# Performance work log

Hardware: AMD Instinct MI355X
Metric: run time of the kernel (lower is better)

The kernel has to match this reference:

```python
import jax, jax.numpy as jnp
import numpy as np
from jax import lax

STRIDE = (1, 1)
PADDING = (1, 1)


def setup_inputs() -> dict:
    key = jax.random.key(0)
    k1, k2 = jax.random.split(key)
    x = jax.random.normal(k1, (32, 128, 56, 56), dtype=jnp.float32)
    kernels = jax.random.normal(k2, (256, 128, 3, 3), dtype=jnp.float32)
    return {"x": x, "kernels": kernels}


def reference(x, kernels):
    # Equivalent to the python-loop correlation conv: NCHW input, OIHW weight,
    # cross-correlation (no kernel flip), stride/padding per module config.
    out = lax.conv_general_dilated(
        x, kernels,
        window_strides=STRIDE,
        padding=[(PADDING[0], PADDING[0]), (PADDING[1], PADDING[1])],
        dimension_numbers=("NCHW", "OIHW", "NCHW"),
    )
    return out
```

## Files before the change

### kernel.cpp

```cpp
#include <hip/hip_runtime.h>
#include <cstdint>

#define N_IMG 32
#define C_IN 128
#define H_IN 56
#define W_IN 56
#define K_OUT 256
#define HW (H_IN * W_IN)
#define M_TOTAL (N_IMG * HW)
#define XP_H 58
#define XP_W 58
#define XP_ELEMS (N_IMG * XP_H * XP_W * C_IN)
#define WT_ELEMS (9 * K_OUT * C_IN)
#define NKT 36

typedef __bf16 bf16x8 __attribute__((ext_vector_type(8)));
typedef float f32x4 __attribute__((ext_vector_type(4)));

__device__ __align__(16) unsigned short g_xp[XP_ELEMS];
__device__ __align__(16) unsigned short g_wt[WT_ELEMS];

static __device__ __forceinline__ unsigned short f2bf(float f) {
    unsigned int u = __builtin_bit_cast(unsigned int, f);
    u += 0x7fffu + ((u >> 16) & 1u);
    return (unsigned short)(u >> 16);
}

static __device__ __forceinline__ void async_copy16(const unsigned short* g, unsigned short* l) {
    auto gp = (const __attribute__((address_space(1))) unsigned int*)g;
    auto lp = (__attribute__((address_space(3))) unsigned int*)l;
    __builtin_amdgcn_global_load_lds(gp, lp, 16, 0, 0);
}

__global__ __launch_bounds__(256) void xpose_x(const float* __restrict__ x) {
    __shared__ float tile[C_IN * 57];
    const int h = blockIdx.x;
    const int n = blockIdx.y;
    const int tid = threadIdx.x;

    if (tid < 32) {
        int col = (tid >> 4) * (XP_W - 1);
        int q = tid & 15;
        uint4* dst = (uint4*)(g_xp + ((size_t)(n * XP_H + h + 1) * XP_W + col) * C_IN) + q;
        *dst = uint4{0u, 0u, 0u, 0u};
    }
    if (h == 0 || h == H_IN - 1) {
        int hp = (h == 0) ? 0 : XP_H - 1;
        uint4* base = (uint4*)(g_xp + ((size_t)(n * XP_H + hp) * XP_W) * C_IN);
        for (int q = tid; q < (XP_W * C_IN) / 8; q += 256) base[q] = uint4{0u, 0u, 0u, 0u};
    }

#pragma unroll
    for (int i = 0; i < 28; i++) {
        int e = i * 256 + tid;
        int c = e / 56;
        int w = e - c * 56;
        tile[c * 57 + w] = x[((n * C_IN + c) * H_IN + h) * W_IN + w];
    }
    __syncthreads();
    unsigned int* outp = (unsigned int*)g_xp;
#pragma unroll
    for (int i = 0; i < 14; i++) {
        int u = i * 256 + tid;
        int w = u >> 6;
        int cp = u & 63;
        float a = tile[(2 * cp) * 57 + w];
        float b = tile[(2 * cp + 1) * 57 + w];
        unsigned int pk = (unsigned int)f2bf(a) | ((unsigned int)f2bf(b) << 16);
        int idx = ((n * XP_H + h + 1) * XP_W + (w + 1)) * C_IN + 2 * cp;
        outp[idx >> 1] = pk;
    }
}

__global__ __launch_bounds__(256) void xpose_w(const float* __restrict__ w) {
    int e = blockIdx.x * 256 + threadIdx.x;
    int rr = e >> 15;
    int rem = e & 32767;
    int k = rem >> 7;
    int c = rem & 127;
    g_wt[e] = f2bf(w[(k * C_IN + c) * 9 + rr]);
}

__global__ __launch_bounds__(512, 4) void conv_main(float* __restrict__ out) {
    __shared__ __align__(16) unsigned short As[3][8192];
    __shared__ __align__(16) unsigned short Bs[3][4096];
    const unsigned short* __restrict__ xp = g_xp;
    const unsigned short* __restrict__ wt = g_wt;

    const int tid = threadIdx.x;
    const int wave = tid >> 6, lane = tid & 63;
    const int lr = lane & 15, lq = lane >> 4;
    const int wmL = (wave >> 1) * 64;
    const int wnL = (wave & 1) * 64;

    const int bid = blockIdx.x;
    const int g = (bid & 7) * 98 + (bid >> 3);
    const int m0 = (g >> 1) * 256;
    const int k0 = (g & 1) * 128;

    int a_src[2], lds_a[2];
#pragma unroll
    for (int j = 0; j < 2; j++) {
        const int su = j * 512 + tid;
        const int row = su >> 2, seg = su & 3;
        const int sw = (seg ^ ((row >> 1) & 3)) * 8;
        int p = m0 + row;
        int n = p / HW;
        int rem = p - n * HW;
        int h = rem / W_IN;
        int w = rem - h * W_IN;
        a_src[j] = ((n * XP_H + h) * XP_W + w) * C_IN + sw;
        lds_a[j] = (j * 512 + wave * 64) * 8;
    }
    const int brow_s = tid >> 2, bseg = tid & 3;
    const int b_src = (k0 + brow_s) * C_IN + (bseg ^ ((brow_s >> 1) & 3)) * 8;
    const int lds_b = wave * 64 * 8;

    const int csw = (lq ^ ((lr >> 1) & 3)) * 8;

    auto stage_tile = [&](int kt, int nb) {
        const int rs = kt >> 2;
        const int r = (rs * 11) >> 5;
        const int sc = rs - r * 3;
        const int aoff = (r * XP_W + sc) * C_IN + (kt & 3) * 32;
        const int boff = rs * (K_OUT * C_IN) + (kt & 3) * 32;
#pragma unroll
        for (int j = 0; j < 2; j++)
            async_copy16(xp + a_src[j] + aoff, &As[nb][lds_a[j]]);
        async_copy16(wt + b_src + boff, &Bs[nb][lds_b]);
    };

    f32x4 acc[4][4];
#pragma unroll
    for (int mi = 0; mi < 4; mi++)
#pragma unroll
        for (int ni = 0; ni < 4; ni++) acc[mi][ni] = f32x4{0.f, 0.f, 0.f, 0.f};

    stage_tile(0, 0);
    stage_tile(1, 1);
    asm volatile("s_waitcnt vmcnt(3)" ::: "memory");
    __builtin_amdgcn_s_barrier();
    asm volatile("" ::: "memory");

    for (int tt = 0; tt < NKT / 3; ++tt) {
#pragma unroll
        for (int u = 0; u < 3; u++) {
            const int t = tt * 3 + u;
            if (t + 2 < NKT) stage_tile(t + 2, (u + 2) % 3);

            bf16x8 af[4], bfv[4];
#pragma unroll
            for (int mi = 0; mi < 4; mi++)
                af[mi] = *(const bf16x8*)(&As[u][(wmL + mi * 16 + lr) * 32 + csw]);
#pragma unroll
            for (int ni = 0; ni < 4; ni++)
                bfv[ni] = *(const bf16x8*)(&Bs[u][(wnL + ni * 16 + lr) * 32 + csw]);
            asm volatile("s_waitcnt lgkmcnt(0)" ::: "memory");
            __builtin_amdgcn_sched_barrier(0);
            __builtin_amdgcn_s_setprio(1);
#pragma unroll
            for (int mi = 0; mi < 4; mi++)
#pragma unroll
                for (int ni = 0; ni < 4; ni++)
                    acc[mi][ni] = __builtin_amdgcn_mfma_f32_16x16x32_bf16(
                        af[mi], bfv[ni], acc[mi][ni], 0, 0, 0);
            __builtin_amdgcn_s_setprio(0);
            if (t + 2 < NKT) {
                asm volatile("s_waitcnt vmcnt(3)" ::: "memory");
            } else {
                asm volatile("s_waitcnt vmcnt(0)" ::: "memory");
            }
            __builtin_amdgcn_s_barrier();
            asm volatile("" ::: "memory");
        }
    }

#pragma unroll
    for (int mi = 0; mi < 4; mi++) {
        int p = m0 + wmL + mi * 16 + lq * 4;
        int n = p / HW;
        int off = p - n * HW;
#pragma unroll
        for (int ni = 0; ni < 4; ni++) {
            int k = k0 + wnL + ni * 16 + lr;
            *(f32x4*)(out + (n * K_OUT + k) * HW + off) = acc[mi][ni];
        }
    }
}

extern "C" void kernel_launch(void* const* d_in, const int* in_sizes, int n_in,
                              void* d_out, int out_size, void* d_ws, size_t ws_size,
                              hipStream_t stream) {
    const float* x = (const float*)d_in[0];
    const float* w = (const float*)d_in[1];
    float* out = (float*)d_out;

    hipLaunchKernelGGL(xpose_x, dim3(H_IN, N_IMG), dim3(256), 0, stream, x);
    hipLaunchKernelGGL(xpose_w, dim3(WT_ELEMS / 256), dim3(256), 0, stream, w);
    hipLaunchKernelGGL(conv_main, dim3((M_TOTAL / 256) * (K_OUT / 128)), dim3(512), 0, stream, out);
}
```

Measured before the change: 239.5 us.

## Stage input halo patch in LDS once and reuse across all filter taps

Each block now loads a 6-row padded NHWC input patch into shared memory once and computes a 224x256 output tile, indexing shifted views of the patch for each of the nine taps. Only the weights are streamed per k-step, through a four-slot async buffer. This removes the repeated global re-fetch of the A operand for every tap and halves the number of blocks covering the channel dimension. In exchange, LDS use grows to roughly 150 KB per block, which lowers occupancy and may leave a wave-quantization tail across the 448 blocks.

Result: faster. 227.9 us (-4.8%).

```diff
diff --git a/kernel.cpp b/kernel.cpp
--- a/kernel.cpp
+++ b/kernel.cpp
@@ -13,6 +13,10 @@
 #define XP_ELEMS (N_IMG * XP_H * XP_W * C_IN)
 #define WT_ELEMS (9 * K_OUT * C_IN)
 #define NKT 36
+#define BM 224
+#define PATCH_PIX (6 * XP_W)
+#define PATCH_SHORTS (PATCH_PIX * C_IN)
+#define PATCH_UNITS (PATCH_SHORTS / 8)
 
 typedef __bf16 bf16x8 __attribute__((ext_vector_type(8)));
 typedef float f32x4 __attribute__((ext_vector_type(4)));
@@ -81,109 +85,111 @@
     g_wt[e] = f2bf(w[(k * C_IN + c) * 9 + rr]);
 }
 
-__global__ __launch_bounds__(512, 4) void conv_main(float* __restrict__ out) {
-    __shared__ __align__(16) unsigned short As[3][8192];
-    __shared__ __align__(16) unsigned short Bs[3][4096];
+__global__ __launch_bounds__(512, 2) void conv_main(float* __restrict__ out) {
+    __shared__ __align__(16) unsigned short patch[PATCH_SHORTS];
+    __shared__ __align__(16) unsigned short Bs[4 * 8192];
     const unsigned short* __restrict__ xp = g_xp;
     const unsigned short* __restrict__ wt = g_wt;
 
     const int tid = threadIdx.x;
     const int wave = tid >> 6, lane = tid & 63;
     const int lr = lane & 15, lq = lane >> 4;
-    const int wmL = (wave >> 1) * 64;
-    const int wnL = (wave & 1) * 64;
+    const int wm0 = (wave & 1) * 112;
+    const int wn0 = (wave >> 1) * 64;
 
     const int bid = blockIdx.x;
-    const int g = (bid & 7) * 98 + (bid >> 3);
-    const int m0 = (g >> 1) * 256;
-    const int k0 = (g & 1) * 128;
-
-    int a_src[2], lds_a[2];
-#pragma unroll
-    for (int j = 0; j < 2; j++) {
-        const int su = j * 512 + tid;
-        const int row = su >> 2, seg = su & 3;
-        const int sw = (seg ^ ((row >> 1) & 3)) * 8;
-        int p = m0 + row;
-        int n = p / HW;
-        int rem = p - n * HW;
-        int h = rem / W_IN;
-        int w = rem - h * W_IN;
-        a_src[j] = ((n * XP_H + h) * XP_W + w) * C_IN + sw;
-        lds_a[j] = (j * 512 + wave * 64) * 8;
-    }
-    const int brow_s = tid >> 2, bseg = tid & 3;
-    const int b_src = (k0 + brow_s) * C_IN + (bseg ^ ((brow_s >> 1) & 3)) * 8;
-    const int lds_b = wave * 64 * 8;
-
-    const int csw = (lq ^ ((lr >> 1) & 3)) * 8;
-
-    auto stage_tile = [&](int kt, int nb) {
-        const int rs = kt >> 2;
-        const int r = (rs * 11) >> 5;
-        const int sc = rs - r * 3;
-        const int aoff = (r * XP_W + sc) * C_IN + (kt & 3) * 32;
-        const int boff = rs * (K_OUT * C_IN) + (kt & 3) * 32;
-#pragma unroll
-        for (int j = 0; j < 2; j++)
-            async_copy16(xp + a_src[j] + aoff, &As[nb][lds_a[j]]);
-        async_copy16(wt + b_src + boff, &Bs[nb][lds_b]);
+    const int gq = (bid & 7) * 56 + (bid >> 3);
+    const int m0 = gq * 224;
+    const int n_img = gq / 14;
+    const int hb = (gq - n_img * 14) * 4;
+
+    int qb[7];
+#pragma unroll
+    for (int mi = 0; mi < 7; mi++) {
+        int pp = wm0 + mi * 16 + lr;
+        qb[mi] = (pp / 56 + 1) * XP_W + (pp % 56 + 1);
+    }
+
+    const int brow = tid >> 2, bsl = tid & 3;
+    const int b_srco  = brow * C_IN + ((bsl ^ ((brow >> 1) & 3)) * 8);
+    const int b_srco2 = (128 + brow) * C_IN + ((bsl ^ (((128 + brow) >> 1) & 3)) * 8);
+    const int b_ldso = wave * 64 * 8;
+
+    auto stage_B = [&](int kt) {
+        const unsigned short* src = wt + (kt >> 2) * (K_OUT * C_IN) + (kt & 3) * 32;
+        unsigned short* dst = &Bs[(kt & 3) * 8192];
+        async_copy16(src + b_srco,  dst + b_ldso);
+        async_copy16(src + b_srco2, dst + 4096 + b_ldso);
     };
 
-    f32x4 acc[4][4];
-#pragma unroll
-    for (int mi = 0; mi < 4; mi++)
-#pragma unroll
-        for (int ni = 0; ni < 4; ni++) acc[mi][ni] = f32x4{0.f, 0.f, 0.f, 0.f};
-
-    stage_tile(0, 0);
-    stage_tile(1, 1);
-    asm volatile("s_waitcnt vmcnt(3)" ::: "memory");
+    const int bswz = (lq ^ ((lr >> 1) & 3)) * 8;
+
+    const size_t srcx = (size_t)(n_img * XP_H + hb) * XP_W * C_IN;
+#pragma unroll
+    for (int i = 0; i < 11; i++) {
+        if (i < 10 || wave < 7) {
+            int u = i * 512 + tid;
+            int ppix = u >> 4, sl = u & 15;
+            async_copy16(xp + srcx + ppix * C_IN + ((sl ^ (ppix & 7)) * 8),
+                         &patch[(i * 512 + wave * 64) * 8]);
+        }
+    }
+    stage_B(0); stage_B(1); stage_B(2);
+    asm volatile("s_waitcnt vmcnt(4)" ::: "memory");
     __builtin_amdgcn_s_barrier();
     asm volatile("" ::: "memory");
 
-    for (int tt = 0; tt < NKT / 3; ++tt) {
-#pragma unroll
-        for (int u = 0; u < 3; u++) {
-            const int t = tt * 3 + u;
-            if (t + 2 < NKT) stage_tile(t + 2, (u + 2) % 3);
-
-            bf16x8 af[4], bfv[4];
-#pragma unroll
-            for (int mi = 0; mi < 4; mi++)
-                af[mi] = *(const bf16x8*)(&As[u][(wmL + mi * 16 + lr) * 32 + csw]);
-#pragma unroll
-            for (int ni = 0; ni < 4; ni++)
-                bfv[ni] = *(const bf16x8*)(&Bs[u][(wnL + ni * 16 + lr) * 32 + csw]);
-            asm volatile("s_waitcnt lgkmcnt(0)" ::: "memory");
-            __builtin_amdgcn_sched_barrier(0);
-            __builtin_amdgcn_s_setprio(1);
-#pragma unroll
-            for (int mi = 0; mi < 4; mi++)
-#pragma unroll
-                for (int ni = 0; ni < 4; ni++)
-                    acc[mi][ni] = __builtin_amdgcn_mfma_f32_16x16x32_bf16(
-                        af[mi], bfv[ni], acc[mi][ni], 0, 0, 0);
-            __builtin_amdgcn_s_setprio(0);
-            if (t + 2 < NKT) {
-                asm volatile("s_waitcnt vmcnt(3)" ::: "memory");
-            } else {
-                asm volatile("s_waitcnt vmcnt(0)" ::: "memory");
-            }
-            __builtin_amdgcn_s_barrier();
-            asm volatile("" ::: "memory");
-        }
-    }
-
-#pragma unroll
-    for (int mi = 0; mi < 4; mi++) {
-        int p = m0 + wmL + mi * 16 + lq * 4;
-        int n = p / HW;
-        int off = p - n * HW;
-#pragma unroll
-        for (int ni = 0; ni < 4; ni++) {
-            int k = k0 + wnL + ni * 16 + lr;
-            *(f32x4*)(out + (n * K_OUT + k) * HW + off) = acc[mi][ni];
+    f32x4 acc[7][4];
+#pragma unroll
+    for (int mi = 0; mi < 7; mi++)
+#pragma unroll
+        for (int nf = 0; nf < 4; nf++) acc[mi][nf] = f32x4{0.f, 0.f, 0.f, 0.f};
+
+    for (int t = 0; t < NKT; ++t) {
+        if (t + 3 < NKT) stage_B(t + 3);
+
+        const int rs = t >> 2;
+        const int r = (rs * 11) >> 5;
+        const int s = rs - r * 3;
+        const int dq = r * XP_W + s - (XP_W + 1);
+        const int so = (t & 3) * 4 + lq;
+
+        bf16x8 bfv[4];
+#pragma unroll
+        for (int nf = 0; nf < 4; nf++)
+            bfv[nf] = *(const bf16x8*)(&Bs[(t & 3) * 8192 + (wn0 + nf * 16 + lr) * 32 + bswz]);
+        bf16x8 af[7];
+#pragma unroll
+        for (int mi = 0; mi < 7; mi++) {
+            int qq = qb[mi] + dq;
+            af[mi] = *(const bf16x8*)(&patch[qq * C_IN + ((so ^ (qq & 7)) * 8)]);
+        }
+#pragma unroll
+        for (int mi = 0; mi < 7; mi++)
+#pragma unroll
+            for (int nf = 0; nf < 4; nf++)
+                acc[mi][nf] = __builtin_amdgcn_mfma_f32_16x16x32_bf16(
+                    af[mi], bfv[nf], acc[mi][nf], 0, 0, 0);
+
+        if (t < NKT - 3) {
+            asm volatile("s_waitcnt vmcnt(4)" ::: "memory");
+        } else if (t == NKT - 3) {
+            asm volatile("s_waitcnt vmcnt(2)" ::: "memory");
+        } else {
+            asm volatile("s_waitcnt vmcnt(0)" ::: "memory");
+        }
+        __builtin_amdgcn_s_barrier();
+        asm volatile("" ::: "memory");
+    }
+
+    const int off0 = m0 - n_img * HW;
+#pragma unroll
+    for (int mi = 0; mi < 7; mi++) {
+        int off = off0 + wm0 + mi * 16 + lq * 4;
+#pragma unroll
+        for (int nf = 0; nf < 4; nf++) {
+            int k = wn0 + nf * 16 + lr;
+            *(f32x4*)(out + ((size_t)(n_img * K_OUT + k)) * HW + off) = acc[mi][nf];
         }
     }
 }
@@ -197,5 +203,5 @@
 
     hipLaunchKernelGGL(xpose_x, dim3(H_IN, N_IMG), dim3(256), 0, stream, x);
     hipLaunchKernelGGL(xpose_w, dim3(WT_ELEMS / 256), dim3(256), 0, stream, w);
-    hipLaunchKernelGGL(conv_main, dim3((M_TOTAL / 256) * (K_OUT / 128)), dim3(512), 0, stream, out);
-}
+    hipLaunchKernelGGL(conv_main, dim3(M_TOTAL / BM), dim3(512), 0, stream, out);
+}
```
